# Optimization experiments

Measured on AMD Instinct MI355X. Metric: run time of the kernel, lower is better.

The kernel has to match this reference:

```python
import jax, jax.numpy as jnp
import numpy as np

B, S, D = 4, 2048, 1024
E, H, K = 8, 2048, 2


def setup_inputs() -> dict:
    key = jax.random.key(0)
    k_x, k_g, k1, k2, k3 = jax.random.split(key, 5)
    x = jax.random.normal(k_x, (B, S, D), dtype=jnp.float32)
    # nn.Linear weight layout is [out, in]
    Wg = jax.random.normal(k_g, (E, D), dtype=jnp.float32) * 0.02   # gate
    W1 = jax.random.normal(k1, (E, H, D), dtype=jnp.float32) * 0.02  # fc1, stacked over experts
    W2 = jax.random.normal(k2, (E, H, D), dtype=jnp.float32) * 0.02  # fc2
    W3 = jax.random.normal(k3, (E, D, H), dtype=jnp.float32) * 0.02  # fc3
    return {"x": x, "Wg": Wg, "W1": W1, "W2": W2, "W3": W3}


def reference(x, Wg, W1, W2, W3):
    # gating
    scores = jnp.einsum("bsd,ed->bse", x, Wg)                 # [B,S,E]
    topk_scores, topk_idx = jax.lax.top_k(scores, K)          # [B,S,K]
    topk_probs = jax.nn.softmax(topk_scores, axis=-1)         # [B,S,K]
    # scatter top-k probs back to a dense [B,S,E] gate (indices are distinct per token)
    gating = jnp.sum(jax.nn.one_hot(topk_idx, E, dtype=x.dtype) * topk_probs[..., None], axis=-2)  # [B,S,E]
    # dense compute-all-experts SwiGLU (faithful to source)
    h1 = jnp.einsum("bsd,ehd->bseh", x, W1)                   # [B,S,E,H]
    h2 = jnp.einsum("bsd,ehd->bseh", x, W2)
    hidden = jax.nn.silu(h1) * h2
    expert_out = jnp.einsum("bseh,edh->bsed", hidden, W3)     # [B,S,E,D]
    y = jnp.einsum("bse,bsed->bsd", gating, expert_out)       # weighted combine
    return y
```

## Files before the change

kernel.cpp:

```cpp
#include <hip/hip_runtime.h>
#include <hip/hip_bf16.h>
#include <cstdint>
#include <cstddef>

typedef unsigned short u16;
typedef uint32_t u32;
typedef __attribute__((ext_vector_type(4))) float f32x4;
typedef __attribute__((ext_vector_type(8))) short bf16x8;

#define NTOK 8192
#define DIM  1024
#define HID  2048
#define NEXP 8
#define MAXT2 136

#define GLD16(g, l) __builtin_amdgcn_global_load_lds( \
    (const __attribute__((address_space(1))) void*)(g), \
    (__attribute__((address_space(3))) void*)(l), 16, 0, 0)

#define WAITV(n) asm volatile("s_waitcnt vmcnt(" #n ")" ::: "memory")

__device__ __forceinline__ u16 f2bf(float f) {
  __hip_bfloat16 h = __float2bfloat16(f);
  return __builtin_bit_cast(u16, h);
}
__device__ __forceinline__ float bf2f(short s) {
  u32 u = ((u32)(u16)s) << 16;
  return __builtin_bit_cast(float, u);
}

__device__ __forceinline__ const bf16x8* lds_frag(const u16* base, int row, int chunk) {
  return (const bf16x8*)(base + row * 64 + ((chunk ^ (row & 7)) << 3));
}

__global__ __launch_bounds__(256) void convert3_kernel(
    const float4* __restrict__ s0, const float4* __restrict__ s1,
    const float4* __restrict__ s2, ushort4* __restrict__ d0,
    ushort4* __restrict__ d1, ushort4* __restrict__ d2) {
  const int n4 = 1 << 22;
  int stride = gridDim.x * blockDim.x;
  for (int i = blockIdx.x * blockDim.x + threadIdx.x; i < 3 * n4; i += stride) {
    int t = i >> 22, off = i & (n4 - 1);
    const float4* s = (t == 0) ? s0 : (t == 1) ? s1 : s2;
    ushort4* d      = (t == 0) ? d0 : (t == 1) ? d1 : d2;
    float4 v = s[off];
    ushort4 o;
    o.x = f2bf(v.x); o.y = f2bf(v.y); o.z = f2bf(v.z); o.w = f2bf(v.w);
    d[off] = o;
  }
}

__global__ __launch_bounds__(256) void gating_kernel(
    const float4* __restrict__ x4, const float4* __restrict__ Wg4,
    int* __restrict__ gate_idx, float* __restrict__ gate_prob,
    u16* __restrict__ Xb) {
  int tid = threadIdx.x, w = tid >> 6, l = tid & 63;
  int t = blockIdx.x * 4 + w;

  float4 xv[4];
#pragma unroll
  for (int j = 0; j < 4; ++j)
    xv[j] = x4[(size_t)t * 256 + l + 64 * j];

  float acc[NEXP];
#pragma unroll
  for (int e = 0; e < NEXP; ++e) acc[e] = 0.f;
#pragma unroll
  for (int e = 0; e < NEXP; ++e)
#pragma unroll
    for (int j = 0; j < 4; ++j) {
      float4 wv = Wg4[e * 256 + l + 64 * j];
      acc[e] += xv[j].x * wv.x + xv[j].y * wv.y + xv[j].z * wv.z + xv[j].w * wv.w;
    }

#pragma unroll
  for (int j = 0; j < 4; ++j) {
    ushort4 o;
    o.x = f2bf(xv[j].x); o.y = f2bf(xv[j].y);
    o.z = f2bf(xv[j].z); o.w = f2bf(xv[j].w);
    *(ushort4*)&Xb[(size_t)t * DIM + (l + 64 * j) * 4] = o;
  }

#pragma unroll
  for (int off = 32; off >= 1; off >>= 1)
#pragma unroll
    for (int e = 0; e < NEXP; ++e)
      acc[e] += __shfl_xor(acc[e], off);

  if (l == 0) {
    float best = -1e30f, sec = -1e30f;
    int bi = 0, si = 0;
#pragma unroll
    for (int e = 0; e < NEXP; ++e) {
      float s = acc[e];
      if (s > best)      { sec = best; si = bi; best = s; bi = e; }
      else if (s > sec)  { sec = s; si = e; }
    }
    float e1  = __expf(sec - best);
    float inv = 1.f / (1.f + e1);
    gate_idx[t * 2]      = bi;
    gate_idx[t * 2 + 1]  = si;
    gate_prob[t * 2]     = inv;
    gate_prob[t * 2 + 1] = e1 * inv;
  }
}

__global__ __launch_bounds__(256) void hist_kernel(
    const int* __restrict__ gate_idx, int* __restrict__ counts) {
  __shared__ int h[NEXP];
  int tid = threadIdx.x;
  if (tid < NEXP) h[tid] = 0;
  __syncthreads();
  int i = blockIdx.x * 256 + tid;
  atomicAdd(&h[gate_idx[i]], 1);
  __syncthreads();
  if (tid < NEXP) atomicAdd(&counts[tid], h[tid]);
}

__global__ void scan_kernel(const int* __restrict__ counts,
                            int* __restrict__ offs, int* __restrict__ cursors,
                            int* __restrict__ tileE2, int* __restrict__ tileRow2,
                            int* __restrict__ nt2) {
  if (threadIdx.x == 0 && blockIdx.x == 0) {
    int s = 0;
    for (int e = 0; e < NEXP; ++e) { offs[e] = s; cursors[e] = s; s += counts[e]; }
    int n2 = 0;
    for (int e = 0; e < NEXP; ++e)
      for (int r = 0; r < counts[e]; r += 128) { tileE2[n2] = e; tileRow2[n2] = r; ++n2; }
    *nt2 = n2;
  }
}

__global__ __launch_bounds__(256) void scatter_kernel(
    const int* __restrict__ gate_idx, int* __restrict__ cursors,
    int* __restrict__ list, int* __restrict__ pos_of) {
  __shared__ int lc[NEXP];
  __shared__ int lbase[NEXP];
  int tid = threadIdx.x;
  if (tid < NEXP) lc[tid] = 0;
  __syncthreads();
  int i = blockIdx.x * 256 + tid;
  int e = gate_idx[i];
  int lp = atomicAdd(&lc[e], 1);
  __syncthreads();
  if (tid < NEXP) lbase[tid] = atomicAdd(&cursors[tid], lc[tid]);
  __syncthreads();
  int pos = lbase[e] + lp;
  list[pos] = i;
  pos_of[i] = pos;
}

__global__ __launch_bounds__(256, 2) void gemm1_kernel(
    const u16* __restrict__ Xb, const u16* __restrict__ W1b,
    const u16* __restrict__ W2b, const int* __restrict__ list,
    const int* __restrict__ offs, const int* __restrict__ counts,
    const int* __restrict__ tileE, const int* __restrict__ tileRow,
    const int* __restrict__ n_tiles, u16* __restrict__ hidden) {
  int flat = blockIdx.x + MAXT2 * blockIdx.y;
  int nf = (flat & 7) * (MAXT2 * (HID / 64) / 8) + (flat >> 3);
  int bx = nf >> 5;
  int tn = nf & 31;
  if (bx >= *n_tiles) return;
  int e = tileE[bx], row0 = tileRow[bx];
  int n_e = counts[e], off_e = offs[e];
  __shared__ u16 As[2][128 * 64];
  __shared__ u16 B1s[2][64 * 64];
  __shared__ u16 B2s[2][64 * 64];
  int tid = threadIdx.x, w = tid >> 6, l = tid & 63;
  const u16* W1e = W1b + (size_t)e * HID * DIM;
  const u16* W2e = W2b + (size_t)e * HID * DIM;

  int schunk = ((l & 7) ^ (l >> 3)) * 8;
  u32 offA[4];
#pragma unroll
  for (int j = 0; j < 4; ++j) {
    int r = w * 32 + j * 8 + (l >> 3);
    int idx = row0 + r;
    int entry = list[off_e + (idx < n_e ? idx : 0)];
    offA[j] = (u32)(entry >> 1) * DIM + schunk;
  }
  u32 offB[2];
#pragma unroll
  for (int j = 0; j < 2; ++j) {
    int r = w * 16 + j * 8 + (l >> 3);
    offB[j] = (u32)(tn * 64 + r) * DIM + schunk;
  }

#define STAGE1(buf, kt) do { u32 kof_ = (u32)(kt) * 64;                        \
    _Pragma("unroll")                                                          \
    for (int j = 0; j < 4; ++j) GLD16(Xb + offA[j] + kof_, &As[buf][w * 2048 + j * 512]); \
    _Pragma("unroll")                                                          \
    for (int j = 0; j < 2; ++j) {                                              \
      GLD16(W1e + offB[j] + kof_, &B1s[buf][w * 1024 + j * 512]);              \
      GLD16(W2e + offB[j] + kof_, &B2s[buf][w * 1024 + j * 512]);              \
    } } while (0)

  f32x4 acc1[4][2], acc2[4][2];
#pragma unroll
  for (int mi = 0; mi < 4; ++mi)
#pragma unroll
    for (int ni = 0; ni < 2; ++ni) {
      acc1[mi][ni] = (f32x4){0.f, 0.f, 0.f, 0.f};
      acc2[mi][ni] = (f32x4){0.f, 0.f, 0.f, 0.f};
    }
  int wm = w >> 1, wn = w & 1;

  STAGE1(0, 0);
  STAGE1(1, 1);
  for (int kt = 0; kt < DIM / 64; ++kt) {
    if (kt < DIM / 64 - 1) { WAITV(8); } else { WAITV(0); }
    __builtin_amdgcn_s_barrier();
    int cur = kt & 1;
    const u16* Ab  = As[cur];
    const u16* B1b = B1s[cur];
    const u16* B2b = B2s[cur];
#pragma unroll
    for (int ks = 0; ks < 2; ++ks) {
      bf16x8 a[4], b1[2], b2[2];
#pragma unroll
      for (int mi = 0; mi < 4; ++mi)
        a[mi] = *lds_frag(Ab, wm * 64 + mi * 16 + (l & 15), ks * 4 + (l >> 4));
#pragma unroll
      for (int ni = 0; ni < 2; ++ni) {
        b1[ni] = *lds_frag(B1b, wn * 32 + ni * 16 + (l & 15), ks * 4 + (l >> 4));
        b2[ni] = *lds_frag(B2b, wn * 32 + ni * 16 + (l & 15), ks * 4 + (l >> 4));
      }
#pragma unroll
      for (int mi = 0; mi < 4; ++mi)
#pragma unroll
        for (int ni = 0; ni < 2; ++ni) {
          acc1[mi][ni] = __builtin_amdgcn_mfma_f32_16x16x32_bf16(a[mi], b1[ni], acc1[mi][ni], 0, 0, 0);
          acc2[mi][ni] = __builtin_amdgcn_mfma_f32_16x16x32_bf16(a[mi], b2[ni], acc2[mi][ni], 0, 0, 0);
        }
    }
    asm volatile("" ::: "memory");
    __builtin_amdgcn_s_barrier();
    if (kt + 2 < DIM / 64) STAGE1(cur, kt + 2);
  }

#pragma unroll
  for (int mi = 0; mi < 4; ++mi) {
#pragma unroll
    for (int i = 0; i < 4; ++i) {
      int m_loc = wm * 64 + mi * 16 + (l >> 4) * 4 + i;
      int idx = row0 + m_loc;
      if (idx < n_e) {
        size_t pos = (size_t)(off_e + idx);
#pragma unroll
        for (int ni = 0; ni < 2; ++ni) {
          int h_loc = tn * 64 + wn * 32 + ni * 16 + (l & 15);
          float h1 = acc1[mi][ni][i];
          float h2 = acc2[mi][ni][i];
          float hv = h1 / (1.f + __expf(-h1)) * h2;
          hidden[pos * HID + h_loc] = f2bf(hv);
        }
      }
    }
  }
#undef STAGE1
}

__global__ __launch_bounds__(256, 2) void gemm2_kernel(
    const u16* __restrict__ hidden, const u16* __restrict__ W3b,
    const int* __restrict__ offs, const int* __restrict__ counts,
    const int* __restrict__ tileE, const int* __restrict__ tileRow,
    const int* __restrict__ n_tiles, u16* __restrict__ eout) {
  int flat = blockIdx.x + MAXT2 * blockIdx.y;
  int nf = (flat & 7) * (MAXT2 * (DIM / 128) / 8) + (flat >> 3);
  int bx = nf >> 3;
  int tn = nf & 7;
  if (bx >= *n_tiles) return;
  int e = tileE[bx], row0 = tileRow[bx];
  int n_e = counts[e], off_e = offs[e];
  __shared__ u16 As[2][128 * 64];
  __shared__ u16 Bs[2][128 * 64];
  int tid = threadIdx.x, w = tid >> 6, l = tid & 63;
  const u16* W3e = W3b + (size_t)e * DIM * HID;

  int schunk = ((l & 7) ^ (l >> 3)) * 8;
  u32 offA[4], offB[4];
#pragma unroll
  for (int j = 0; j < 4; ++j) {
    int r = w * 32 + j * 8 + (l >> 3);
    int idx = row0 + r;
    int pos = off_e + (idx < n_e ? idx : 0);
    offA[j] = (u32)pos * HID + schunk;
    offB[j] = (u32)(tn * 128 + r) * HID + schunk;
  }

#define STAGE2(buf, kt) do { u32 kof_ = (u32)(kt) * 64;                        \
    _Pragma("unroll")                                                          \
    for (int j = 0; j < 4; ++j) {                                              \
      GLD16(hidden + offA[j] + kof_, &As[buf][w * 2048 + j * 512]);            \
      GLD16(W3e    + offB[j] + kof_, &Bs[buf][w * 2048 + j * 512]);            \
    } } while (0)

  f32x4 acc[4][4];
#pragma unroll
  for (int mi = 0; mi < 4; ++mi)
#pragma unroll
    for (int ni = 0; ni < 4; ++ni) acc[mi][ni] = (f32x4){0.f, 0.f, 0.f, 0.f};
  int wm = w >> 1, wn = w & 1;

  STAGE2(0, 0);
  STAGE2(1, 1);
  for (int kt = 0; kt < HID / 64; ++kt) {
    if (kt < HID / 64 - 1) { WAITV(8); } else { WAITV(0); }
    __builtin_amdgcn_s_barrier();
    int cur = kt & 1;
    const u16* Ab = As[cur];
    const u16* Bb = Bs[cur];
#pragma unroll
    for (int ks = 0; ks < 2; ++ks) {
      bf16x8 a[4], b[4];
#pragma unroll
      for (int mi = 0; mi < 4; ++mi)
        a[mi] = *lds_frag(Ab, wm * 64 + mi * 16 + (l & 15), ks * 4 + (l >> 4));
#pragma unroll
      for (int ni = 0; ni < 4; ++ni)
        b[ni] = *lds_frag(Bb, wn * 64 + ni * 16 + (l & 15), ks * 4 + (l >> 4));
#pragma unroll
      for (int mi = 0; mi < 4; ++mi)
#pragma unroll
        for (int ni = 0; ni < 4; ++ni)
          acc[mi][ni] = __builtin_amdgcn_mfma_f32_16x16x32_bf16(a[mi], b[ni], acc[mi][ni], 0, 0, 0);
    }
    asm volatile("" ::: "memory");
    __builtin_amdgcn_s_barrier();
    if (kt + 2 < HID / 64) STAGE2(cur, kt + 2);
  }

#pragma unroll
  for (int mi = 0; mi < 4; ++mi) {
#pragma unroll
    for (int i = 0; i < 4; ++i) {
      int m_loc = wm * 64 + mi * 16 + (l >> 4) * 4 + i;
      int idx = row0 + m_loc;
      if (idx < n_e) {
        size_t pos = (size_t)(off_e + idx);
#pragma unroll
        for (int ni = 0; ni < 4; ++ni) {
          int d_loc = tn * 128 + wn * 64 + ni * 16 + (l & 15);
          eout[pos * DIM + d_loc] = f2bf(acc[mi][ni][i]);
        }
      }
    }
  }
#undef STAGE2
}

__global__ __launch_bounds__(256) void combine_kernel(
    const u16* __restrict__ eout, const int* __restrict__ pos_of,
    const float* __restrict__ gate_prob, float* __restrict__ out) {
  int gid = blockIdx.x * 256 + threadIdx.x;
  int t = gid >> 7, dq = (gid & 127) * 8;
  int p0 = pos_of[t * 2], p1 = pos_of[t * 2 + 1];
  float w0 = gate_prob[t * 2], w1 = gate_prob[t * 2 + 1];
  bf16x8 e0 = *(const bf16x8*)&eout[(size_t)p0 * DIM + dq];
  bf16x8 e1 = *(const bf16x8*)&eout[(size_t)p1 * DIM + dq];
  float4 o0, o1;
  o0.x = w0 * bf2f(e0[0]) + w1 * bf2f(e1[0]);
  o0.y = w0 * bf2f(e0[1]) + w1 * bf2f(e1[1]);
  o0.z = w0 * bf2f(e0[2]) + w1 * bf2f(e1[2]);
  o0.w = w0 * bf2f(e0[3]) + w1 * bf2f(e1[3]);
  o1.x = w0 * bf2f(e0[4]) + w1 * bf2f(e1[4]);
  o1.y = w0 * bf2f(e0[5]) + w1 * bf2f(e1[5]);
  o1.z = w0 * bf2f(e0[6]) + w1 * bf2f(e1[6]);
  o1.w = w0 * bf2f(e0[7]) + w1 * bf2f(e1[7]);
  float4* op = (float4*)&out[(size_t)t * DIM + dq];
  op[0] = o0; op[1] = o1;
}

extern "C" void kernel_launch(void* const* d_in, const int* in_sizes, int n_in,
                              void* d_out, int out_size, void* d_ws, size_t ws_size,
                              hipStream_t stream) {
  const float* x  = (const float*)d_in[0];
  const float* Wg = (const float*)d_in[1];
  const float* W1 = (const float*)d_in[2];
  const float* W2 = (const float*)d_in[3];
  const float* W3 = (const float*)d_in[4];
  float* out = (float*)d_out;

  char* wsb = (char*)d_ws;
  int*   counts    = (int*)(wsb + 0);
  int*   cursors   = (int*)(wsb + 64);
  int*   offs      = (int*)(wsb + 128);
  int*   nt2       = (int*)(wsb + 196);
  int*   tileE2    = (int*)(wsb + 1536);
  int*   tileRow2  = (int*)(wsb + 2560);
  int*   gate_idx  = (int*)(wsb + 4096);
  float* gate_prob = (float*)(wsb + 4096 + 65536);
  int*   pos_of    = (int*)(wsb + 4096 + 2 * 65536);
  int*   list      = (int*)(wsb + 4096 + 3 * 65536);
  u16* Xb     = (u16*)(wsb + (1 << 20));
  u16* W1b    = Xb  + (size_t)NTOK * DIM;
  u16* W2b    = W1b + (size_t)NEXP * HID * DIM;
  u16* W3b    = W2b + (size_t)NEXP * HID * DIM;
  u16* hidden = W3b + (size_t)NEXP * DIM * HID;
  u16* eout   = W1b;

  hipMemsetAsync(wsb, 0, 256, stream);

  convert3_kernel<<<4096, 256, 0, stream>>>(
      (const float4*)W1, (const float4*)W2, (const float4*)W3,
      (ushort4*)W1b, (ushort4*)W2b, (ushort4*)W3b);

  gating_kernel<<<NTOK / 4, 256, 0, stream>>>(
      (const float4*)x, (const float4*)Wg, gate_idx, gate_prob, Xb);
  hist_kernel<<<NTOK * 2 / 256, 256, 0, stream>>>(gate_idx, counts);
  scan_kernel<<<1, 64, 0, stream>>>(counts, offs, cursors, tileE2, tileRow2, nt2);
  scatter_kernel<<<NTOK * 2 / 256, 256, 0, stream>>>(gate_idx, cursors, list, pos_of);

  gemm1_kernel<<<dim3(MAXT2, HID / 64), 256, 0, stream>>>(
      Xb, W1b, W2b, list, offs, counts, tileE2, tileRow2, nt2, hidden);
  gemm2_kernel<<<dim3(MAXT2, DIM / 128), 256, 0, stream>>>(
      hidden, W3b, offs, counts, tileE2, tileRow2, nt2, eout);
  combine_kernel<<<NTOK * 128 / 256, 256, 0, stream>>>(eout, pos_of, gate_prob, out);
}
```

Measured before the change: 362.5 us.

## Fuse prep kernels with gating histogram and restructure GEMM k-loop prefetch

Merges the weight conversion, gating and histogram into one launch: the first 2048 blocks do gating and atomically count expert assignments into padded counters, and the remaining blocks convert the weights. This removes two launches and one pass over gate_idx. Both grouped GEMMs now read all LDS fragments for a k-tile into registers first, then wait on LDS, barrier, issue the next global-to-LDS prefetch, and run the MFMAs. This lets the prefetch overlap the math, at the cost of more registers held per k-step and an extra barrier.

```diff
diff --git a/kernel.cpp b/kernel.cpp
--- a/kernel.cpp
+++ b/kernel.cpp
@@ -19,6 +19,8 @@
     (__attribute__((address_space(3))) void*)(l), 16, 0, 0)
 
 #define WAITV(n) asm volatile("s_waitcnt vmcnt(" #n ")" ::: "memory")
+#define WAITL(n) asm volatile("s_waitcnt lgkmcnt(" #n ")" ::: "memory")
+#define SFENCE() __builtin_amdgcn_sched_barrier(0)
 
 __device__ __forceinline__ u16 f2bf(float f) {
   __hip_bfloat16 h = __float2bfloat16(f);
@@ -33,100 +35,96 @@
   return (const bf16x8*)(base + row * 64 + ((chunk ^ (row & 7)) << 3));
 }
 
-__global__ __launch_bounds__(256) void convert3_kernel(
+__global__ __launch_bounds__(256) void prep_kernel(
+    const float4* __restrict__ x4, const float4* __restrict__ Wg4,
     const float4* __restrict__ s0, const float4* __restrict__ s1,
     const float4* __restrict__ s2, ushort4* __restrict__ d0,
-    ushort4* __restrict__ d1, ushort4* __restrict__ d2) {
-  const int n4 = 1 << 22;
-  int stride = gridDim.x * blockDim.x;
-  for (int i = blockIdx.x * blockDim.x + threadIdx.x; i < 3 * n4; i += stride) {
-    int t = i >> 22, off = i & (n4 - 1);
-    const float4* s = (t == 0) ? s0 : (t == 1) ? s1 : s2;
-    ushort4* d      = (t == 0) ? d0 : (t == 1) ? d1 : d2;
-    float4 v = s[off];
-    ushort4 o;
-    o.x = f2bf(v.x); o.y = f2bf(v.y); o.z = f2bf(v.z); o.w = f2bf(v.w);
-    d[off] = o;
-  }
-}
-
-__global__ __launch_bounds__(256) void gating_kernel(
-    const float4* __restrict__ x4, const float4* __restrict__ Wg4,
+    ushort4* __restrict__ d1, ushort4* __restrict__ d2,
     int* __restrict__ gate_idx, float* __restrict__ gate_prob,
-    u16* __restrict__ Xb) {
-  int tid = threadIdx.x, w = tid >> 6, l = tid & 63;
-  int t = blockIdx.x * 4 + w;
-
-  float4 xv[4];
-#pragma unroll
-  for (int j = 0; j < 4; ++j)
-    xv[j] = x4[(size_t)t * 256 + l + 64 * j];
-
-  float acc[NEXP];
-#pragma unroll
-  for (int e = 0; e < NEXP; ++e) acc[e] = 0.f;
-#pragma unroll
-  for (int e = 0; e < NEXP; ++e)
+    u16* __restrict__ Xb, int* __restrict__ counts_pad) {
+  int tid = threadIdx.x;
+  if (blockIdx.x < 2048) {
+    int w = tid >> 6, l = tid & 63;
+    int t = blockIdx.x * 4 + w;
+
+    float4 xv[4];
+#pragma unroll
+    for (int j = 0; j < 4; ++j)
+      xv[j] = x4[(size_t)t * 256 + l + 64 * j];
+
+    float acc[NEXP];
+#pragma unroll
+    for (int e = 0; e < NEXP; ++e) acc[e] = 0.f;
+#pragma unroll
+    for (int e = 0; e < NEXP; ++e)
+#pragma unroll
+      for (int j = 0; j < 4; ++j) {
+        float4 wv = Wg4[e * 256 + l + 64 * j];
+        acc[e] += xv[j].x * wv.x + xv[j].y * wv.y + xv[j].z * wv.z + xv[j].w * wv.w;
+      }
+
 #pragma unroll
     for (int j = 0; j < 4; ++j) {
-      float4 wv = Wg4[e * 256 + l + 64 * j];
-      acc[e] += xv[j].x * wv.x + xv[j].y * wv.y + xv[j].z * wv.z + xv[j].w * wv.w;
-    }
-
-#pragma unroll
-  for (int j = 0; j < 4; ++j) {
-    ushort4 o;
-    o.x = f2bf(xv[j].x); o.y = f2bf(xv[j].y);
-    o.z = f2bf(xv[j].z); o.w = f2bf(xv[j].w);
-    *(ushort4*)&Xb[(size_t)t * DIM + (l + 64 * j) * 4] = o;
-  }
-
-#pragma unroll
-  for (int off = 32; off >= 1; off >>= 1)
-#pragma unroll
-    for (int e = 0; e < NEXP; ++e)
-      acc[e] += __shfl_xor(acc[e], off);
-
-  if (l == 0) {
-    float best = -1e30f, sec = -1e30f;
-    int bi = 0, si = 0;
-#pragma unroll
-    for (int e = 0; e < NEXP; ++e) {
-      float s = acc[e];
-      if (s > best)      { sec = best; si = bi; best = s; bi = e; }
-      else if (s > sec)  { sec = s; si = e; }
-    }
-    float e1  = __expf(sec - best);
-    float inv = 1.f / (1.f + e1);
-    gate_idx[t * 2]      = bi;
-    gate_idx[t * 2 + 1]  = si;
-    gate_prob[t * 2]     = inv;
-    gate_prob[t * 2 + 1] = e1 * inv;
-  }
-}
-
-__global__ __launch_bounds__(256) void hist_kernel(
-    const int* __restrict__ gate_idx, int* __restrict__ counts) {
-  __shared__ int h[NEXP];
-  int tid = threadIdx.x;
-  if (tid < NEXP) h[tid] = 0;
-  __syncthreads();
-  int i = blockIdx.x * 256 + tid;
-  atomicAdd(&h[gate_idx[i]], 1);
-  __syncthreads();
-  if (tid < NEXP) atomicAdd(&counts[tid], h[tid]);
-}
-
-__global__ void scan_kernel(const int* __restrict__ counts,
+      ushort4 o;
+      o.x = f2bf(xv[j].x); o.y = f2bf(xv[j].y);
+      o.z = f2bf(xv[j].z); o.w = f2bf(xv[j].w);
+      *(ushort4*)&Xb[(size_t)t * DIM + (l + 64 * j) * 4] = o;
+    }
+
+#pragma unroll
+    for (int off = 32; off >= 1; off >>= 1)
+#pragma unroll
+      for (int e = 0; e < NEXP; ++e)
+        acc[e] += __shfl_xor(acc[e], off);
+
+    if (l == 0) {
+      float best = -1e30f, sec = -1e30f;
+      int bi = 0, si = 0;
+#pragma unroll
+      for (int e = 0; e < NEXP; ++e) {
+        float s = acc[e];
+        if (s > best)      { sec = best; si = bi; best = s; bi = e; }
+        else if (s > sec)  { sec = s; si = e; }
+      }
+      float e1  = __expf(sec - best);
+      float inv = 1.f / (1.f + e1);
+      gate_idx[t * 2]      = bi;
+      gate_idx[t * 2 + 1]  = si;
+      gate_prob[t * 2]     = inv;
+      gate_prob[t * 2 + 1] = e1 * inv;
+      atomicAdd(&counts_pad[bi * 16], 1);
+      atomicAdd(&counts_pad[si * 16], 1);
+    }
+  } else {
+    const int n4 = 1 << 22;
+    int stride = (gridDim.x - 2048) * 256;
+    for (int i = (blockIdx.x - 2048) * 256 + tid; i < 3 * n4; i += stride) {
+      int t = i >> 22, off = i & (n4 - 1);
+      const float4* s = (t == 0) ? s0 : (t == 1) ? s1 : s2;
+      ushort4* d      = (t == 0) ? d0 : (t == 1) ? d1 : d2;
+      float4 v = s[off];
+      ushort4 o;
+      o.x = f2bf(v.x); o.y = f2bf(v.y); o.z = f2bf(v.z); o.w = f2bf(v.w);
+      d[off] = o;
+    }
+  }
+}
+
+__global__ void scan_kernel(const int* __restrict__ counts_pad,
+                            int* __restrict__ counts_c,
                             int* __restrict__ offs, int* __restrict__ cursors,
                             int* __restrict__ tileE2, int* __restrict__ tileRow2,
                             int* __restrict__ nt2) {
   if (threadIdx.x == 0 && blockIdx.x == 0) {
     int s = 0;
-    for (int e = 0; e < NEXP; ++e) { offs[e] = s; cursors[e] = s; s += counts[e]; }
+    for (int e = 0; e < NEXP; ++e) {
+      int c = counts_pad[e * 16];
+      counts_c[e] = c;
+      offs[e] = s; cursors[e] = s; s += c;
+    }
     int n2 = 0;
     for (int e = 0; e < NEXP; ++e)
-      for (int r = 0; r < counts[e]; r += 128) { tileE2[n2] = e; tileRow2[n2] = r; ++n2; }
+      for (int r = 0; r < counts_c[e]; r += 128) { tileE2[n2] = e; tileRow2[n2] = r; ++n2; }
     *nt2 = n2;
   }
 }
@@ -205,37 +203,46 @@
     }
   int wm = w >> 1, wn = w & 1;
 
+  const int NKT = DIM / 64;
   STAGE1(0, 0);
   STAGE1(1, 1);
-  for (int kt = 0; kt < DIM / 64; ++kt) {
-    if (kt < DIM / 64 - 1) { WAITV(8); } else { WAITV(0); }
-    __builtin_amdgcn_s_barrier();
+  WAITV(8);
+  __builtin_amdgcn_s_barrier();
+
+  for (int kt = 0; kt < NKT; ++kt) {
     int cur = kt & 1;
     const u16* Ab  = As[cur];
     const u16* B1b = B1s[cur];
     const u16* B2b = B2s[cur];
+    bf16x8 a[2][4], b1[2][2], b2[2][2];
 #pragma unroll
     for (int ks = 0; ks < 2; ++ks) {
-      bf16x8 a[4], b1[2], b2[2];
 #pragma unroll
       for (int mi = 0; mi < 4; ++mi)
-        a[mi] = *lds_frag(Ab, wm * 64 + mi * 16 + (l & 15), ks * 4 + (l >> 4));
+        a[ks][mi] = *lds_frag(Ab, wm * 64 + mi * 16 + (l & 15), ks * 4 + (l >> 4));
 #pragma unroll
       for (int ni = 0; ni < 2; ++ni) {
-        b1[ni] = *lds_frag(B1b, wn * 32 + ni * 16 + (l & 15), ks * 4 + (l >> 4));
-        b2[ni] = *lds_frag(B2b, wn * 32 + ni * 16 + (l & 15), ks * 4 + (l >> 4));
+        b1[ks][ni] = *lds_frag(B1b, wn * 32 + ni * 16 + (l & 15), ks * 4 + (l >> 4));
+        b2[ks][ni] = *lds_frag(B2b, wn * 32 + ni * 16 + (l & 15), ks * 4 + (l >> 4));
       }
+    }
+    WAITL(0);
+    __builtin_amdgcn_s_barrier();
+    if (kt + 2 < NKT) STAGE1(cur, kt + 2);
+    SFENCE();
+#pragma unroll
+    for (int ks = 0; ks < 2; ++ks)
 #pragma unroll
       for (int mi = 0; mi < 4; ++mi)
 #pragma unroll
         for (int ni = 0; ni < 2; ++ni) {
-          acc1[mi][ni] = __builtin_amdgcn_mfma_f32_16x16x32_bf16(a[mi], b1[ni], acc1[mi][ni], 0, 0, 0);
-          acc2[mi][ni] = __builtin_amdgcn_mfma_f32_16x16x32_bf16(a[mi], b2[ni], acc2[mi][ni], 0, 0, 0);
+          acc1[mi][ni] = __builtin_amdgcn_mfma_f32_16x16x32_bf16(a[ks][mi], b1[ks][ni], acc1[mi][ni], 0, 0, 0);
+          acc2[mi][ni] = __builtin_amdgcn_mfma_f32_16x16x32_bf16(a[ks][mi], b2[ks][ni], acc2[mi][ni], 0, 0, 0);
         }
-    }
-    asm volatile("" ::: "memory");
-    __builtin_amdgcn_s_barrier();
-    if (kt + 2 < DIM / 64) STAGE1(cur, kt + 2);
+    if (kt + 1 < NKT) {
+      if (kt + 2 < NKT) { WAITV(8); } else { WAITV(0); }
+      __builtin_amdgcn_s_barrier();
+    }
   }
 
 #pragma unroll
@@ -302,32 +309,41 @@
     for (int ni = 0; ni < 4; ++ni) acc[mi][ni] = (f32x4){0.f, 0.f, 0.f, 0.f};
   int wm = w >> 1, wn = w & 1;
 
+  const int NKT = HID / 64;
   STAGE2(0, 0);
   STAGE2(1, 1);
-  for (int kt = 0; kt < HID / 64; ++kt) {
-    if (kt < HID / 64 - 1) { WAITV(8); } else { WAITV(0); }
-    __builtin_amdgcn_s_barrier();
+  WAITV(8);
+  __builtin_amdgcn_s_barrier();
+
+  for (int kt = 0; kt < NKT; ++kt) {
     int cur = kt & 1;
     const u16* Ab = As[cur];
     const u16* Bb = Bs[cur];
+    bf16x8 a[2][4], b[2][4];
 #pragma unroll
     for (int ks = 0; ks < 2; ++ks) {
-      bf16x8 a[4], b[4];
 #pragma unroll
       for (int mi = 0; mi < 4; ++mi)
-        a[mi] = *lds_frag(Ab, wm * 64 + mi * 16 + (l & 15), ks * 4 + (l >> 4));
+        a[ks][mi] = *lds_frag(Ab, wm * 64 + mi * 16 + (l & 15), ks * 4 + (l >> 4));
 #pragma unroll
       for (int ni = 0; ni < 4; ++ni)
-        b[ni] = *lds_frag(Bb, wn * 64 + ni * 16 + (l & 15), ks * 4 + (l >> 4));
+        b[ks][ni] = *lds_frag(Bb, wn * 64 + ni * 16 + (l & 15), ks * 4 + (l >> 4));
+    }
+    WAITL(0);
+    __builtin_amdgcn_s_barrier();
+    if (kt + 2 < NKT) STAGE2(cur, kt + 2);
+    SFENCE();
+#pragma unroll
+    for (int ks = 0; ks < 2; ++ks)
 #pragma unroll
       for (int mi = 0; mi < 4; ++mi)
 #pragma unroll
         for (int ni = 0; ni < 4; ++ni)
-          acc[mi][ni] = __builtin_amdgcn_mfma_f32_16x16x32_bf16(a[mi], b[ni], acc[mi][ni], 0, 0, 0);
-    }
-    asm volatile("" ::: "memory");
-    __builtin_amdgcn_s_barrier();
-    if (kt + 2 < HID / 64) STAGE2(cur, kt + 2);
+          acc[mi][ni] = __builtin_amdgcn_mfma_f32_16x16x32_bf16(a[ks][mi], b[ks][ni], acc[mi][ni], 0, 0, 0);
+    if (kt + 1 < NKT) {
+      if (kt + 2 < NKT) { WAITV(8); } else { WAITV(0); }
+      __builtin_amdgcn_s_barrier();
+    }
   }
 
 #pragma unroll
@@ -382,16 +398,17 @@
   float* out = (float*)d_out;
 
   char* wsb = (char*)d_ws;
-  int*   counts    = (int*)(wsb + 0);
-  int*   cursors   = (int*)(wsb + 64);
-  int*   offs      = (int*)(wsb + 128);
-  int*   nt2       = (int*)(wsb + 196);
-  int*   tileE2    = (int*)(wsb + 1536);
-  int*   tileRow2  = (int*)(wsb + 2560);
-  int*   gate_idx  = (int*)(wsb + 4096);
-  float* gate_prob = (float*)(wsb + 4096 + 65536);
-  int*   pos_of    = (int*)(wsb + 4096 + 2 * 65536);
-  int*   list      = (int*)(wsb + 4096 + 3 * 65536);
+  int*   counts_pad = (int*)(wsb + 0);
+  int*   cursors    = (int*)(wsb + 512);
+  int*   offs       = (int*)(wsb + 576);
+  int*   nt2        = (int*)(wsb + 640);
+  int*   counts_c   = (int*)(wsb + 704);
+  int*   tileE2     = (int*)(wsb + 1024);
+  int*   tileRow2   = (int*)(wsb + 2048);
+  int*   gate_idx   = (int*)(wsb + 4096);
+  float* gate_prob  = (float*)(wsb + 4096 + 65536);
+  int*   pos_of     = (int*)(wsb + 4096 + 2 * 65536);
+  int*   list       = (int*)(wsb + 4096 + 3 * 65536);
   u16* Xb     = (u16*)(wsb + (1 << 20));
   u16* W1b    = Xb  + (size_t)NTOK * DIM;
   u16* W2b    = W1b + (size_t)NEXP * HID * DIM;
@@ -399,21 +416,20 @@
   u16* hidden = W3b + (size_t)NEXP * DIM * HID;
   u16* eout   = W1b;
 
-  hipMemsetAsync(wsb, 0, 256, stream);
-
-  convert3_kernel<<<4096, 256, 0, stream>>>(
+  hipMemsetAsync(wsb, 0, 1024, stream);
+
+  prep_kernel<<<6144, 256, 0, stream>>>(
+      (const float4*)x, (const float4*)Wg,
       (const float4*)W1, (const float4*)W2, (const float4*)W3,
-      (ushort4*)W1b, (ushort4*)W2b, (ushort4*)W3b);
-
-  gating_kernel<<<NTOK / 4, 256, 0, stream>>>(
-      (const float4*)x, (const float4*)Wg, gate_idx, gate_prob, Xb);
-  hist_kernel<<<NTOK * 2 / 256, 256, 0, stream>>>(gate_idx, counts);
-  scan_kernel<<<1, 64, 0, stream>>>(counts, offs, cursors, tileE2, tileRow2, nt2);
+      (ushort4*)W1b, (ushort4*)W2b, (ushort4*)W3b,
+      gate_idx, gate_prob, Xb, counts_pad);
+  scan_kernel<<<1, 64, 0, stream>>>(counts_pad, counts_c, offs, cursors,
+                                    tileE2, tileRow2, nt2);
   scatter_kernel<<<NTOK * 2 / 256, 256, 0, stream>>>(gate_idx, cursors, list, pos_of);
 
   gemm1_kernel<<<dim3(MAXT2, HID / 64), 256, 0, stream>>>(
-      Xb, W1b, W2b, list, offs, counts, tileE2, tileRow2, nt2, hidden);
+      Xb, W1b, W2b, list, offs, counts_c, tileE2, tileRow2, nt2, hidden);
   gemm2_kernel<<<dim3(MAXT2, DIM / 128), 256, 0, stream>>>(
-      hidden, W3b, offs, counts, tileE2, tileRow2, nt2, eout);
+      hidden, W3b, offs, counts_c, tileE2, tileRow2, nt2, eout);
   combine_kernel<<<NTOK * 128 / 256, 256, 0, stream>>>(eout, pos_of, gate_prob, out);
 }
```

Result: slower. 392.4 us (+8.3%).
